# Kernel tuning notes

Hardware: AMD Instinct MI355X
Metric: run time of the kernel (lower is better)

## Reference

```python
import jax, jax.numpy as jnp
import numpy as np

A_NUM = 9
C_NUM = 20

def setup_inputs() -> dict:
    key = jax.random.key(0)
    ks = jax.random.split(key, 12)
    B, Cin, H, W = 32, 256, 56, 56
    hidden = 256
    N, M = 64, 2048
    out_ch = 5 * A_NUM + C_NUM
    features = jax.random.normal(ks[0], (B, Cin, H, W), jnp.float32)
    w1 = jax.random.normal(ks[1], (hidden, Cin), jnp.float32) * (1.0 / np.sqrt(Cin))
    b1 = jax.random.normal(ks[2], (hidden,), jnp.float32) * 0.01
    w2 = jax.random.normal(ks[3], (out_ch, hidden), jnp.float32) * (1.0 / np.sqrt(hidden))
    b2 = jax.random.normal(ks[4], (out_ch,), jnp.float32) * 0.01
    # anchor shapes (w, h), positive sizes in grid units
    anc = 1.0 + 5.0 * jax.random.uniform(ks[5], (A_NUM, 2), jnp.float32)
    # grid of cell centers
    xs = jnp.arange(W, dtype=jnp.float32) + 0.5
    ys = jnp.arange(H, dtype=jnp.float32) + 0.5
    gx, gy = jnp.meshgrid(xs, ys, indexing='xy')  # (H, W)
    grid = jnp.broadcast_to(jnp.stack([gx, gy], axis=-1)[None], (B, H, W, 2))
    # GT boxes (x1, y1, x2, y2, cls) with x1<x2, y1<y2
    x1 = jax.random.uniform(ks[6], (B, N), jnp.float32) * (W - 9.0)
    y1 = jax.random.uniform(ks[7], (B, N), jnp.float32) * (H - 9.0)
    bw = 1.0 + 7.0 * jax.random.uniform(ks[8], (B, N), jnp.float32)
    bh = 1.0 + 7.0 * jax.random.uniform(ks[9], (B, N), jnp.float32)
    cls = jax.random.randint(ks[10], (B, N), 0, C_NUM).astype(jnp.float32)
    bboxes = jnp.stack([x1, y1, x1 + bw, y1 + bh, cls], axis=-1)
    total_anchors = B * A_NUM * H * W
    pos_anchor_idx = jax.random.randint(ks[11], (M,), 0, total_anchors, jnp.int64 if jax.config.jax_enable_x64 else jnp.int32)
    neg_anchor_idx = jax.random.randint(jax.random.fold_in(key, 99), (M,), 0, total_anchors, jnp.int64 if jax.config.jax_enable_x64 else jnp.int32)
    GT_offsets = jax.random.normal(jax.random.fold_in(key, 100), (M, 4), jnp.float32) * 0.1
    return {"features": features, "w1": w1, "b1": b1, "w2": w2, "b2": b2,
            "anc": anc, "grid": grid, "bboxes": bboxes, "GT_offsets": GT_offsets,
            "pos_anchor_idx": pos_anchor_idx, "neg_anchor_idx": neg_anchor_idx}

def _generate_anchor(anc, grid):
    # grid: (B,H,W,2), anc: (A,2) -> anchors (B,A,H,W,4) as (x1,y1,x2,y2)
    g = grid[:, None]                      # (B,1,H,W,2)
    a = anc[None, :, None, None]           # (1,A,1,1,2)
    return jnp.concatenate([g - a / 2, g + a / 2], axis=-1)

def _generate_proposal_yolo(anchors, offsets):
    ctr = (anchors[..., :2] + anchors[..., 2:]) / 2
    wh = anchors[..., 2:] - anchors[..., :2]
    new_wh = wh * jnp.exp(offsets[..., 2:])
    new_ctr = ctr + offsets[..., :2]
    return jnp.concatenate([new_ctr - new_wh / 2, new_ctr + new_wh / 2], axis=-1)

def _iou(proposals, bboxes):
    # proposals (B,A,H,W,4) -> (B,AHW,4); bboxes (B,N,5) -> iou (B,AHW,N)
    B = proposals.shape[0]
    p = proposals.reshape(B, -1, 4)[:, :, None, :]   # (B,AHW,1,4)
    g = bboxes[:, None, :, :]                        # (B,1,N,5)
    ix1 = jnp.maximum(p[..., 0], g[..., 0])
    iy1 = jnp.maximum(p[..., 1], g[..., 1])
    ix2 = jnp.minimum(p[..., 2], g[..., 2])
    iy2 = jnp.minimum(p[..., 3], g[..., 3])
    inter = jnp.clip(ix2 - ix1, 0) * jnp.clip(iy2 - iy1, 0)
    gt_area = (bboxes[:, :, 2] - bboxes[:, :, 0]) * (bboxes[:, :, 3] - bboxes[:, :, 1])
    p_area = (p[..., 2] - p[..., 0]) * (p[..., 3] - p[..., 1])
    return inter / (gt_area[:, None, :] + p_area - inter)

def reference(features, w1, b1, w2, b2, anc, grid, bboxes, GT_offsets,
              pos_anchor_idx, neg_anchor_idx):
    B, _, H, W = features.shape
    A = anc.shape[0]
    M = pos_anchor_idx.shape[0]
    # PredictionNetwork (dropout in eval = identity), 1x1 convs as einsum
    x = jnp.einsum('bchw,oc->bohw', features, w1) + b1[None, :, None, None]
    x = jax.nn.leaky_relu(x, 0.01)
    x = jnp.einsum('bchw,oc->bohw', x, w2) + b2[None, :, None, None]
    anc_data = x[:, :5 * A].reshape(B, A, 5, H, W)
    class_all = x[:, 5 * A:]                               # (B,C,H,W)
    conf_all = jax.nn.sigmoid(anc_data[:, :, 0])           # (B,A,H,W)
    offsets_all = jnp.transpose(anc_data[:, :, 1:5], (0, 1, 3, 4, 2))  # (B,A,H,W,4)
    # training extraction
    conf_flat = conf_all.reshape(-1)
    conf_scores = jnp.concatenate([conf_flat[pos_anchor_idx], conf_flat[neg_anchor_idx]])[:, None]  # (2M,1)
    offsets_pos = offsets_all.reshape(-1, 4)[pos_anchor_idx]            # (M,4)
    # class scores for positive anchors: index arithmetic over (B,A,H,W)
    bi = pos_anchor_idx // (A * H * W)
    hw = pos_anchor_idx % (H * W)
    hi, wi = hw // W, hw % W
    class_pos = class_all[bi, :, hi, wi]                                # (M,C)
    # anchors -> proposals -> IoU
    anchors = _generate_anchor(anc, grid)
    proposals = _generate_proposal_yolo(anchors, offsets_all)
    iou_mat = _iou(proposals, bboxes)                                   # (B,AHW,N)
    # YOLO SSE losses
    gt_conf = jnp.concatenate([jnp.ones((M, 1), conf_scores.dtype), jnp.zeros((M, 1), conf_scores.dtype)])
    conf_loss = jnp.sum((conf_scores - gt_conf) ** 2) / (2 * M)
    reg_loss = jnp.sum((offsets_pos - GT_offsets) ** 2) / M
    total_loss = conf_loss + reg_loss
    return total_loss, iou_mat, class_pos
```

## Files before the change

kernel.cpp:

```cpp
#include <hip/hip_runtime.h>
#include <math.h>

#define B_    32
#define CIN   256
#define HID   256
#define OC    65
#define A_    9
#define H_    56
#define W_    56
#define HW    3136
#define AHW   28224
#define NBOX  64
#define M_    2048
#define CNUM  20
#define NTILE 49

#define IOU_N ((size_t)B_ * AHW * NBOX)

#define FOFF(frag) (((frag) << 3) + ((((frag) >> 3)) << 3))

typedef _Float16 half8 __attribute__((ext_vector_type(8)));
typedef float f32x16 __attribute__((ext_vector_type(16)));
typedef float f32x4  __attribute__((ext_vector_type(4)));

__device__ __forceinline__ unsigned int pkh(float a, float b) {
    _Float16 ha = (_Float16)a, hb = (_Float16)b;
    unsigned short ua = __builtin_bit_cast(unsigned short, ha);
    unsigned short ub = __builtin_bit_cast(unsigned short, hb);
    return (unsigned int)ua | ((unsigned int)ub << 16);
}

__global__ __launch_bounds__(256) void prep_kernel(
    const float* __restrict__ w1, const float* __restrict__ w2,
    _Float16* __restrict__ w1s, _Float16* __restrict__ w2s,
    float* __restrict__ loss_ws)
{
    const int f = blockIdx.x * 256 + threadIdx.x;
    if (f < 2) loss_ws[f] = 0.f;
    {
        const int e    = f & 7;
        const int lane = (f >> 3) & 63;
        const int kc   = (f >> 9) & 15;
        const int ob   = f >> 13;
        const int row  = ob * 32 + (lane & 31);
        const int k    = kc * 16 + (lane >> 5) * 8 + e;
        w1s[f] = (_Float16)w1[row * CIN + k];
    }
    if (f < 20480) {
        const int e    = f & 7;
        const int lane = (f >> 3) & 63;
        const int ks2  = (f >> 9) & 7;
        const int rt   = f >> 12;
        const int row  = rt * 16 + (lane & 15);
        const int k    = ks2 * 32 + (lane >> 4) * 8 + e;
        w2s[f] = (row < OC) ? (_Float16)w2[row * HID + k] : (_Float16)0.f;
    }
}

__global__ __launch_bounds__(256) void conv_iou_kernel(
    const float* __restrict__ features, const _Float16* __restrict__ w1s,
    const float* __restrict__ b1, const _Float16* __restrict__ w2s,
    const float* __restrict__ b2, const float* __restrict__ anc,
    const float* __restrict__ bboxes, const int* __restrict__ pos_idx,
    const int* __restrict__ neg_idx, const float* __restrict__ gt_off,
    float* __restrict__ iou_out, float* __restrict__ cls_out,
    float* __restrict__ loss_ws)
{
    __shared__ _Float16 lds_h[18432];
    __shared__ float bias_s[HID];
    __shared__ float boxs[5 * 64];
    __shared__ float red[8];

    _Float16* featAll = lds_h;
    _Float16* hidf    = lds_h;
    float*    L       = (float*)lds_h;
    float*    x2t     = L;
    float*    ppx1    = L + 4416;
    float*    ppy1    = L + 4992;
    float*    ppx2    = L + 5568;
    float*    ppy2    = L + 6144;
    float*    pare    = L + 6720;

    const int t    = threadIdx.x;
    const int lane = t & 63;
    const int w    = t >> 6;
    const int bid  = blockIdx.x;
    const int b    = bid / NTILE;
    const int p0   = (bid - b * NTILE) * 64;
    const float* fbase = features + (size_t)b * CIN * HW + p0;

    bias_s[t] = b1[t];
    if (t < 64) {
        const float* gb = bboxes + ((size_t)b * NBOX + t) * 5;
        const float x1 = gb[0], y1 = gb[1], x2v = gb[2], y2v = gb[3];
        boxs[t] = x1; boxs[64 + t] = y1; boxs[128 + t] = x2v; boxs[192 + t] = y2v;
        boxs[256 + t] = (x2v - x1) * (y2v - y1);
    }

    const int pstage = (t & 15) * 4;
    const int kk     = (t >> 4) * 2;
    const int ksS    = kk >> 4;
    const int gS     = (kk >> 3) & 1;
    const int j0h    = kk & 7;
    const int ghalf  = lane >> 5;

#pragma unroll
    for (int c = 0; c < 8; ++c) {
        const float4 r0 = *(const float4*)(fbase + (size_t)(c * 32 + kk) * HW + pstage);
        const float4 r1 = *(const float4*)(fbase + (size_t)(c * 32 + kk + 1) * HW + pstage);
        const float a0[4] = {r0.x, r0.y, r0.z, r0.w};
        const float a1[4] = {r1.x, r1.y, r1.z, r1.w};
#pragma unroll
        for (int e = 0; e < 4; ++e) {
            const int p     = pstage + e;
            const int lane2 = gS * 32 + (p & 31);
            const int pt    = p >> 5;
            const int frag  = c * 256 + (ksS * 2 + pt) * 64 + lane2;
            *(unsigned int*)&featAll[FOFF(frag) + j0h] = pkh(a0[e], a1[e]);
        }
    }
    __syncthreads();

    f32x16 facc[2][2];
#pragma unroll
    for (int ot = 0; ot < 2; ++ot)
#pragma unroll
        for (int pt = 0; pt < 2; ++pt)
#pragma unroll
            for (int e = 0; e < 16; ++e) facc[ot][pt][e] = 0.f;

    half8 afb[2][2][2];
#pragma unroll
    for (int ks = 0; ks < 2; ++ks)
#pragma unroll
        for (int ot = 0; ot < 2; ++ot)
            afb[0][ks][ot] = *(const half8*)(w1s + ((size_t)((w * 2 + ot) * 16 + ks) * 64 + lane) * 8);

#pragma unroll
    for (int c = 0; c < 8; ++c) {
        if (c < 7) {
#pragma unroll
            for (int ks = 0; ks < 2; ++ks)
#pragma unroll
                for (int ot = 0; ot < 2; ++ot)
                    afb[(c + 1) & 1][ks][ot] =
                        *(const half8*)(w1s + ((size_t)((w * 2 + ot) * 16 + (c + 1) * 2 + ks) * 64 + lane) * 8);
        }
#pragma unroll
        for (int ks = 0; ks < 2; ++ks) {
#pragma unroll
            for (int pt = 0; pt < 2; ++pt) {
                const half8 bf = *(const half8*)&featAll[FOFF(c * 256 + (ks * 2 + pt) * 64 + lane)];
                facc[0][pt] = __builtin_amdgcn_mfma_f32_32x32x16_f16(afb[c & 1][ks][0], bf, facc[0][pt], 0, 0, 0);
                facc[1][pt] = __builtin_amdgcn_mfma_f32_32x32x16_f16(afb[c & 1][ks][1], bf, facc[1][pt], 0, 0, 0);
            }
        }
    }
    __syncthreads();

    const int col = lane & 31;
#pragma unroll
    for (int ot = 0; ot < 2; ++ot) {
        const int ks2 = w * 2 + ot;
#pragma unroll
        for (int pt = 0; pt < 2; ++pt) {
            const int pt2 = pt * 2 + (col >> 4);
            const int n15 = col & 15;
#pragma unroll
            for (int q = 0; q < 4; ++q) {
                float hv[4];
#pragma unroll
                for (int i = 0; i < 4; ++i) {
                    const int row = i + 8 * q + 4 * ghalf;
                    float v = facc[ot][pt][q * 4 + i] + bias_s[w * 64 + ot * 32 + row];
                    hv[i] = v < 0.f ? 0.01f * v : v;
                }
                const int frag = (ks2 * 4 + pt2) * 64 + (q * 16 + n15);
                *(unsigned int*)&hidf[FOFF(frag) + 4 * ghalf]     = pkh(hv[0], hv[1]);
                *(unsigned int*)&hidf[FOFF(frag) + 4 * ghalf + 2] = pkh(hv[2], hv[3]);
            }
        }
    }
    __syncthreads();

    f32x4 c2[5];
#pragma unroll
    for (int rt = 0; rt < 5; ++rt)
#pragma unroll
        for (int e = 0; e < 4; ++e) c2[rt][e] = 0.f;

    const int m16 = lane & 15;
    const int kgr = lane >> 4;
#pragma unroll 2
    for (int ks2 = 0; ks2 < 8; ++ks2) {
        const half8 bf = *(const half8*)&hidf[FOFF((ks2 * 4 + w) * 64 + lane)];
#pragma unroll
        for (int rt = 0; rt < 5; ++rt) {
            const half8 af = *(const half8*)(w2s + ((size_t)(rt * 8 + ks2) * 64 + lane) * 8);
            c2[rt] = __builtin_amdgcn_mfma_f32_16x16x32_f16(af, bf, c2[rt], 0, 0, 0);
        }
    }
    __syncthreads();

    const int pxl = w * 16 + m16;
#pragma unroll
    for (int rt = 0; rt < 5; ++rt) {
#pragma unroll
        for (int r = 0; r < 4; ++r) {
            const int o2 = rt * 16 + kgr * 4 + r;
            if (o2 < OC) x2t[pxl * 69 + o2] = c2[rt][r] + b2[o2];
        }
    }
    __syncthreads();

    for (int pi = t; pi < A_ * 64; pi += 256) {
        const int a  = pi >> 6;
        const int px = pi & 63;
        const float* xr = x2t + px * 69 + 5 * a;
        const float tx = xr[1], ty = xr[2], tw = xr[3], th = xr[4];
        const int hw = p0 + px;
        const int h  = hw / W_;
        const int wv = hw - h * W_;
        const float gx = (float)wv + 0.5f;
        const float gy = (float)h + 0.5f;
        const float nw = anc[2 * a]     * __expf(tw);
        const float nh = anc[2 * a + 1] * __expf(th);
        const float cx = gx + tx, cy = gy + ty;
        ppx1[pi] = cx - 0.5f * nw; ppy1[pi] = cy - 0.5f * nh;
        ppx2[pi] = cx + 0.5f * nw; ppy2[pi] = cy + 0.5f * nh;
        pare[pi] = nw * nh;
    }
    __syncthreads();

    const int pr = lane >> 4;
    const int j0 = (lane & 15) * 4;
    float Bx1[4], By1[4], Bx2[4], By2[4], Ba[4];
#pragma unroll
    for (int e = 0; e < 4; ++e) {
        Bx1[e] = boxs[j0 + e];       By1[e] = boxs[64 + j0 + e];
        Bx2[e] = boxs[128 + j0 + e]; By2[e] = boxs[192 + j0 + e];
        Ba[e]  = boxs[256 + j0 + e];
    }
    float* ibase = iou_out + ((size_t)b * AHW + p0) * 64;
#pragma unroll 1
    for (int a = 0; a < A_; ++a) {
#pragma unroll
        for (int q = 0; q < 4; ++q) {
            const int p = w * 16 + q * 4 + pr;
            const int i = a * 64 + p;
            const float Px1 = ppx1[i], Py1 = ppy1[i], Px2 = ppx2[i], Py2 = ppy2[i];
            const float pa = pare[i];
            f32x4 o4;
#pragma unroll
            for (int e = 0; e < 4; ++e) {
                const float iw = fminf(Px2, Bx2[e]) - fmaxf(Px1, Bx1[e]);
                const float ih = fminf(Py2, By2[e]) - fmaxf(Py1, By1[e]);
                const float inter = fmaxf(iw, 0.f) * fmaxf(ih, 0.f);
                o4[e] = inter * __builtin_amdgcn_rcpf(Ba[e] + pa - inter);
            }
            __builtin_nontemporal_store(o4, (f32x4*)(ibase + ((size_t)a * HW + p) * 64 + j0));
        }
    }

    float csum = 0.f, rsum = 0.f;
    for (int m = t; m < M_; m += 256) {
        const int idx = pos_idx[m];
        const int bi  = idx / AHW;
        const int rr  = idx - bi * AHW;
        const int a   = rr / HW;
        const int px  = (rr - a * HW) - p0;
        if (bi == b && px >= 0 && px < 64) {
            const float* xr = x2t + px * 69;
            const float s = 1.f / (1.f + __expf(-xr[5 * a]));
            csum += (s - 1.f) * (s - 1.f);
#pragma unroll
            for (int k = 0; k < 4; ++k) {
                const float d = xr[5 * a + 1 + k] - gt_off[m * 4 + k];
                rsum += d * d;
            }
            float* co = cls_out + (size_t)m * CNUM;
#pragma unroll
            for (int c = 0; c < CNUM; ++c) co[c] = xr[45 + c];
        }
    }
    for (int m = t; m < M_; m += 256) {
        const int idx = neg_idx[m];
        const int bi  = idx / AHW;
        const int rr  = idx - bi * AHW;
        const int a   = rr / HW;
        const int px  = (rr - a * HW) - p0;
        if (bi == b && px >= 0 && px < 64) {
            const float s = 1.f / (1.f + __expf(-x2t[px * 69 + 5 * a]));
            csum += s * s;
        }
    }
#pragma unroll
    for (int off = 32; off > 0; off >>= 1) {
        csum += __shfl_down(csum, off, 64);
        rsum += __shfl_down(rsum, off, 64);
    }
    if (lane == 0) { red[w] = csum; red[4 + w] = rsum; }
    __syncthreads();
    if (t == 0) {
        const float c  = red[0] + red[1] + red[2] + red[3];
        const float rg = red[4] + red[5] + red[6] + red[7];
        if (c != 0.f || rg != 0.f) {
            atomicAdd(&loss_ws[0], c);
            atomicAdd(&loss_ws[1], rg);
        }
    }
}

__global__ void finalize_kernel(const float* __restrict__ loss_ws, float* __restrict__ out0)
{
    out0[0] = loss_ws[0] / (2.f * (float)M_) + loss_ws[1] / (float)M_;
}

extern "C" void kernel_launch(void* const* d_in, const int* in_sizes, int n_in,
                              void* d_out, int out_size, void* d_ws, size_t ws_size,
                              hipStream_t stream) {
    (void)in_sizes; (void)n_in; (void)out_size; (void)ws_size;
    const float* features = (const float*)d_in[0];
    const float* w1       = (const float*)d_in[1];
    const float* b1       = (const float*)d_in[2];
    const float* w2       = (const float*)d_in[3];
    const float* b2       = (const float*)d_in[4];
    const float* anc      = (const float*)d_in[5];
    const float* bboxes   = (const float*)d_in[7];
    const float* gt_off   = (const float*)d_in[8];
    const int*   pos_idx  = (const int*)d_in[9];
    const int*   neg_idx  = (const int*)d_in[10];
    float* out = (float*)d_out;

    char* wsb = (char*)d_ws;
    _Float16* w1s  = (_Float16*)wsb;
    _Float16* w2s  = w1s + 65536;
    float* loss_ws = (float*)(wsb + 131072 + 40960);

    prep_kernel<<<256, 256, 0, stream>>>(w1, w2, w1s, w2s, loss_ws);
    conv_iou_kernel<<<B_ * NTILE, 256, 0, stream>>>(features, w1s, b1, w2s, b2,
                                                    anc, bboxes, pos_idx, neg_idx,
                                                    gt_off, out + 1,
                                                    out + 1 + IOU_N, loss_ws);
    finalize_kernel<<<1, 1, 0, stream>>>(loss_ws, out);
}
```

Baseline: 379.4 us.

## Split IoU computation into separate kernel with proposals staged in workspace

Moves the IoU matrix generation out of the fused conv kernel into its own kernel launched over batch×anchor×tile blocks, with proposal boxes written to a workspace buffer in planar layout. The intent is to spread the large IoU output write across many more blocks (more memory-level parallelism) instead of 1568 blocks each serially writing nine anchor slices. It adds a kernel launch and an extra global round-trip of proposal data, and requires the workspace to hold five planes of B*A*HW floats.

```diff
diff --git a/kernel.cpp b/kernel.cpp
--- a/kernel.cpp
+++ b/kernel.cpp
@@ -15,6 +15,7 @@
 #define CNUM  20
 #define NTILE 49
 
+#define PLANE ((size_t)B_ * A_ * HW)
 #define IOU_N ((size_t)B_ * AHW * NBOX)
 
 #define FOFF(frag) (((frag) << 3) + ((((frag) >> 3)) << 3))
@@ -57,29 +58,23 @@
     }
 }
 
-__global__ __launch_bounds__(256) void conv_iou_kernel(
+__global__ __launch_bounds__(256) void conv_kernel(
     const float* __restrict__ features, const _Float16* __restrict__ w1s,
     const float* __restrict__ b1, const _Float16* __restrict__ w2s,
     const float* __restrict__ b2, const float* __restrict__ anc,
-    const float* __restrict__ bboxes, const int* __restrict__ pos_idx,
-    const int* __restrict__ neg_idx, const float* __restrict__ gt_off,
-    float* __restrict__ iou_out, float* __restrict__ cls_out,
+    const int* __restrict__ pos_idx, const int* __restrict__ neg_idx,
+    const float* __restrict__ gt_off,
+    float* __restrict__ prop, float* __restrict__ cls_out,
     float* __restrict__ loss_ws)
 {
     __shared__ _Float16 lds_h[18432];
     __shared__ float bias_s[HID];
-    __shared__ float boxs[5 * 64];
     __shared__ float red[8];
 
     _Float16* featAll = lds_h;
     _Float16* hidf    = lds_h;
     float*    L       = (float*)lds_h;
     float*    x2t     = L;
-    float*    ppx1    = L + 4416;
-    float*    ppy1    = L + 4992;
-    float*    ppx2    = L + 5568;
-    float*    ppy2    = L + 6144;
-    float*    pare    = L + 6720;
 
     const int t    = threadIdx.x;
     const int lane = t & 63;
@@ -90,12 +85,6 @@
     const float* fbase = features + (size_t)b * CIN * HW + p0;
 
     bias_s[t] = b1[t];
-    if (t < 64) {
-        const float* gb = bboxes + ((size_t)b * NBOX + t) * 5;
-        const float x1 = gb[0], y1 = gb[1], x2v = gb[2], y2v = gb[3];
-        boxs[t] = x1; boxs[64 + t] = y1; boxs[128 + t] = x2v; boxs[192 + t] = y2v;
-        boxs[256 + t] = (x2v - x1) * (y2v - y1);
-    }
 
     const int pstage = (t & 15) * 4;
     const int kk     = (t >> 4) * 2;
@@ -226,40 +215,12 @@
         const float nw = anc[2 * a]     * __expf(tw);
         const float nh = anc[2 * a + 1] * __expf(th);
         const float cx = gx + tx, cy = gy + ty;
-        ppx1[pi] = cx - 0.5f * nw; ppy1[pi] = cy - 0.5f * nh;
-        ppx2[pi] = cx + 0.5f * nw; ppy2[pi] = cy + 0.5f * nh;
-        pare[pi] = nw * nh;
-    }
-    __syncthreads();
-
-    const int pr = lane >> 4;
-    const int j0 = (lane & 15) * 4;
-    float Bx1[4], By1[4], Bx2[4], By2[4], Ba[4];
-#pragma unroll
-    for (int e = 0; e < 4; ++e) {
-        Bx1[e] = boxs[j0 + e];       By1[e] = boxs[64 + j0 + e];
-        Bx2[e] = boxs[128 + j0 + e]; By2[e] = boxs[192 + j0 + e];
-        Ba[e]  = boxs[256 + j0 + e];
-    }
-    float* ibase = iou_out + ((size_t)b * AHW + p0) * 64;
-#pragma unroll 1
-    for (int a = 0; a < A_; ++a) {
-#pragma unroll
-        for (int q = 0; q < 4; ++q) {
-            const int p = w * 16 + q * 4 + pr;
-            const int i = a * 64 + p;
-            const float Px1 = ppx1[i], Py1 = ppy1[i], Px2 = ppx2[i], Py2 = ppy2[i];
-            const float pa = pare[i];
-            f32x4 o4;
-#pragma unroll
-            for (int e = 0; e < 4; ++e) {
-                const float iw = fminf(Px2, Bx2[e]) - fmaxf(Px1, Bx1[e]);
-                const float ih = fminf(Py2, By2[e]) - fmaxf(Py1, By1[e]);
-                const float inter = fmaxf(iw, 0.f) * fmaxf(ih, 0.f);
-                o4[e] = inter * __builtin_amdgcn_rcpf(Ba[e] + pa - inter);
-            }
-            __builtin_nontemporal_store(o4, (f32x4*)(ibase + ((size_t)a * HW + p) * 64 + j0));
-        }
+        const size_t pb = ((size_t)b * A_ + a) * HW + p0 + px;
+        prop[pb]             = cx - 0.5f * nw;
+        prop[PLANE + pb]     = cy - 0.5f * nh;
+        prop[2 * PLANE + pb] = cx + 0.5f * nw;
+        prop[3 * PLANE + pb] = cy + 0.5f * nh;
+        prop[4 * PLANE + pb] = nw * nh;
     }
 
     float csum = 0.f, rsum = 0.f;
@@ -308,6 +269,64 @@
             atomicAdd(&loss_ws[0], c);
             atomicAdd(&loss_ws[1], rg);
         }
+    }
+}
+
+__global__ __launch_bounds__(256) void iou_kernel(
+    const float* __restrict__ prop, const float* __restrict__ bboxes,
+    float* __restrict__ iou_out)
+{
+    __shared__ float P[5 * 64];
+    __shared__ float boxs[5 * 64];
+
+    const int t    = threadIdx.x;
+    const int lane = t & 63;
+    const int w    = t >> 6;
+    const int bid  = blockIdx.x;
+    const int b    = bid / (A_ * NTILE);
+    const int r    = bid - b * (A_ * NTILE);
+    const int a    = r / NTILE;
+    const int p0   = (r - a * NTILE) * 64;
+
+    const size_t pbase = ((size_t)b * A_ + a) * HW + p0;
+
+    if (t < 64) {
+        const float* gb = bboxes + ((size_t)b * NBOX + t) * 5;
+        const float x1 = gb[0], y1 = gb[1], x2v = gb[2], y2v = gb[3];
+        boxs[t] = x1; boxs[64 + t] = y1; boxs[128 + t] = x2v; boxs[192 + t] = y2v;
+        boxs[256 + t] = (x2v - x1) * (y2v - y1);
+    }
+    for (int i = t; i < 320; i += 256) {
+        const int s = i >> 6;
+        P[i] = prop[(size_t)s * PLANE + pbase + (i & 63)];
+    }
+    __syncthreads();
+
+    const int pr = lane >> 4;
+    const int j0 = (lane & 15) * 4;
+    float Bx1[4], By1[4], Bx2[4], By2[4], Ba[4];
+#pragma unroll
+    for (int e = 0; e < 4; ++e) {
+        Bx1[e] = boxs[j0 + e];       By1[e] = boxs[64 + j0 + e];
+        Bx2[e] = boxs[128 + j0 + e]; By2[e] = boxs[192 + j0 + e];
+        Ba[e]  = boxs[256 + j0 + e];
+    }
+
+    float* ibase = iou_out + pbase * 64;
+#pragma unroll
+    for (int q = 0; q < 4; ++q) {
+        const int p = w * 16 + q * 4 + pr;
+        const float Px1 = P[p], Py1 = P[64 + p], Px2 = P[128 + p], Py2 = P[192 + p];
+        const float pa  = P[256 + p];
+        f32x4 o4;
+#pragma unroll
+        for (int e = 0; e < 4; ++e) {
+            const float iw = fminf(Px2, Bx2[e]) - fmaxf(Px1, Bx1[e]);
+            const float ih = fminf(Py2, By2[e]) - fmaxf(Py1, By1[e]);
+            const float inter = fmaxf(iw, 0.f) * fmaxf(ih, 0.f);
+            o4[e] = inter * __builtin_amdgcn_rcpf(Ba[e] + pa - inter);
+        }
+        __builtin_nontemporal_store(o4, (f32x4*)(ibase + (size_t)p * 64 + j0));
     }
 }
 
@@ -336,11 +355,12 @@
     _Float16* w1s  = (_Float16*)wsb;
     _Float16* w2s  = w1s + 65536;
     float* loss_ws = (float*)(wsb + 131072 + 40960);
+    float* prop    = (float*)(wsb + 172288);
 
     prep_kernel<<<256, 256, 0, stream>>>(w1, w2, w1s, w2s, loss_ws);
-    conv_iou_kernel<<<B_ * NTILE, 256, 0, stream>>>(features, w1s, b1, w2s, b2,
-                                                    anc, bboxes, pos_idx, neg_idx,
-                                                    gt_off, out + 1,
-                                                    out + 1 + IOU_N, loss_ws);
+    conv_kernel<<<B_ * NTILE, 256, 0, stream>>>(features, w1s, b1, w2s, b2, anc,
+                                                pos_idx, neg_idx, gt_off,
+                                                prop, out + 1 + IOU_N, loss_ws);
+    iou_kernel<<<B_ * A_ * NTILE, 256, 0, stream>>>(prop, bboxes, out + 1);
     finalize_kernel<<<1, 1, 0, stream>>>(loss_ws, out);
 }
```

Result: slower. 389.9 us (+2.8%).

## Make each wave own 16 pixels end-to-end, removing shared staging and block barriers

Applied to the files above, without the earlier changes.

The first 1x1 conv now uses 16x16x32 MFMAs. Each wave loads its own 16 pixels of features straight into registers, so the shared-memory feature staging is gone. Every later stage (hidden activations, head output, proposals, IoU) uses per-wave LDS regions, which removes most __syncthreads between stages. The LDS footprint shrinks and launch bounds request 3 blocks per CU to raise occupancy. The trade-off is strided scalar global loads for features, 16 accumulator tiles per wave that increase register pressure, and IoU stores that are no longer nontemporal.

```diff
diff --git a/kernel.cpp b/kernel.cpp
--- a/kernel.cpp
+++ b/kernel.cpp
@@ -17,10 +17,7 @@
 
 #define IOU_N ((size_t)B_ * AHW * NBOX)
 
-#define FOFF(frag) (((frag) << 3) + ((((frag) >> 3)) << 3))
-
 typedef _Float16 half8 __attribute__((ext_vector_type(8)));
-typedef float f32x16 __attribute__((ext_vector_type(16)));
 typedef float f32x4  __attribute__((ext_vector_type(4)));
 
 __device__ __forceinline__ unsigned int pkh(float a, float b) {
@@ -40,10 +37,10 @@
     {
         const int e    = f & 7;
         const int lane = (f >> 3) & 63;
-        const int kc   = (f >> 9) & 15;
-        const int ob   = f >> 13;
-        const int row  = ob * 32 + (lane & 31);
-        const int k    = kc * 16 + (lane >> 5) * 8 + e;
+        const int ks   = (f >> 9) & 7;
+        const int rt   = (f >> 12) & 15;
+        const int row  = rt * 16 + (lane & 15);
+        const int k    = ks * 32 + (lane >> 4) * 8 + e;
         w1s[f] = (_Float16)w1[row * CIN + k];
     }
     if (f < 20480) {
@@ -57,7 +54,7 @@
     }
 }
 
-__global__ __launch_bounds__(256) void conv_iou_kernel(
+__global__ __launch_bounds__(256, 3) void conv_iou_kernel(
     const float* __restrict__ features, const _Float16* __restrict__ w1s,
     const float* __restrict__ b1, const _Float16* __restrict__ w2s,
     const float* __restrict__ b2, const float* __restrict__ anc,
@@ -66,122 +63,67 @@
     float* __restrict__ iou_out, float* __restrict__ cls_out,
     float* __restrict__ loss_ws)
 {
-    __shared__ _Float16 lds_h[18432];
-    __shared__ float bias_s[HID];
-    __shared__ float boxs[5 * 64];
+    __shared__ _Float16 lds_h[16384];
     __shared__ float red[8];
 
-    _Float16* featAll = lds_h;
-    _Float16* hidf    = lds_h;
-    float*    L       = (float*)lds_h;
-    float*    x2t     = L;
-    float*    ppx1    = L + 4416;
-    float*    ppy1    = L + 4992;
-    float*    ppx2    = L + 5568;
-    float*    ppy2    = L + 6144;
-    float*    pare    = L + 6720;
+    float* LF = (float*)lds_h;
 
     const int t    = threadIdx.x;
     const int lane = t & 63;
     const int w    = t >> 6;
+    const int pxw  = lane & 15;
+    const int g    = lane >> 4;
     const int bid  = blockIdx.x;
     const int b    = bid / NTILE;
     const int p0   = (bid - b * NTILE) * 64;
-    const float* fbase = features + (size_t)b * CIN * HW + p0;
-
-    bias_s[t] = b1[t];
-    if (t < 64) {
-        const float* gb = bboxes + ((size_t)b * NBOX + t) * 5;
-        const float x1 = gb[0], y1 = gb[1], x2v = gb[2], y2v = gb[3];
-        boxs[t] = x1; boxs[64 + t] = y1; boxs[128 + t] = x2v; boxs[192 + t] = y2v;
-        boxs[256 + t] = (x2v - x1) * (y2v - y1);
-    }
-
-    const int pstage = (t & 15) * 4;
-    const int kk     = (t >> 4) * 2;
-    const int ksS    = kk >> 4;
-    const int gS     = (kk >> 3) & 1;
-    const int j0h    = kk & 7;
-    const int ghalf  = lane >> 5;
-
-#pragma unroll
-    for (int c = 0; c < 8; ++c) {
-        const float4 r0 = *(const float4*)(fbase + (size_t)(c * 32 + kk) * HW + pstage);
-        const float4 r1 = *(const float4*)(fbase + (size_t)(c * 32 + kk + 1) * HW + pstage);
-        const float a0[4] = {r0.x, r0.y, r0.z, r0.w};
-        const float a1[4] = {r1.x, r1.y, r1.z, r1.w};
-#pragma unroll
-        for (int e = 0; e < 4; ++e) {
-            const int p     = pstage + e;
-            const int lane2 = gS * 32 + (p & 31);
-            const int pt    = p >> 5;
-            const int frag  = c * 256 + (ksS * 2 + pt) * 64 + lane2;
-            *(unsigned int*)&featAll[FOFF(frag) + j0h] = pkh(a0[e], a1[e]);
-        }
-    }
-    __syncthreads();
-
-    f32x16 facc[2][2];
-#pragma unroll
-    for (int ot = 0; ot < 2; ++ot)
-#pragma unroll
-        for (int pt = 0; pt < 2; ++pt)
-#pragma unroll
-            for (int e = 0; e < 16; ++e) facc[ot][pt][e] = 0.f;
-
-    half8 afb[2][2][2];
-#pragma unroll
-    for (int ks = 0; ks < 2; ++ks)
-#pragma unroll
-        for (int ot = 0; ot < 2; ++ot)
-            afb[0][ks][ot] = *(const half8*)(w1s + ((size_t)((w * 2 + ot) * 16 + ks) * 64 + lane) * 8);
-
-#pragma unroll
-    for (int c = 0; c < 8; ++c) {
-        if (c < 7) {
-#pragma unroll
-            for (int ks = 0; ks < 2; ++ks)
-#pragma unroll
-                for (int ot = 0; ot < 2; ++ot)
-                    afb[(c + 1) & 1][ks][ot] =
-                        *(const half8*)(w1s + ((size_t)((w * 2 + ot) * 16 + (c + 1) * 2 + ks) * 64 + lane) * 8);
-        }
-#pragma unroll
-        for (int ks = 0; ks < 2; ++ks) {
-#pragma unroll
-            for (int pt = 0; pt < 2; ++pt) {
-                const half8 bf = *(const half8*)&featAll[FOFF(c * 256 + (ks * 2 + pt) * 64 + lane)];
-                facc[0][pt] = __builtin_amdgcn_mfma_f32_32x32x16_f16(afb[c & 1][ks][0], bf, facc[0][pt], 0, 0, 0);
-                facc[1][pt] = __builtin_amdgcn_mfma_f32_32x32x16_f16(afb[c & 1][ks][1], bf, facc[1][pt], 0, 0, 0);
-            }
-        }
-    }
-    __syncthreads();
-
-    const int col = lane & 31;
-#pragma unroll
-    for (int ot = 0; ot < 2; ++ot) {
-        const int ks2 = w * 2 + ot;
-#pragma unroll
-        for (int pt = 0; pt < 2; ++pt) {
-            const int pt2 = pt * 2 + (col >> 4);
-            const int n15 = col & 15;
-#pragma unroll
-            for (int q = 0; q < 4; ++q) {
-                float hv[4];
-#pragma unroll
-                for (int i = 0; i < 4; ++i) {
-                    const int row = i + 8 * q + 4 * ghalf;
-                    float v = facc[ot][pt][q * 4 + i] + bias_s[w * 64 + ot * 32 + row];
-                    hv[i] = v < 0.f ? 0.01f * v : v;
-                }
-                const int frag = (ks2 * 4 + pt2) * 64 + (q * 16 + n15);
-                *(unsigned int*)&hidf[FOFF(frag) + 4 * ghalf]     = pkh(hv[0], hv[1]);
-                *(unsigned int*)&hidf[FOFF(frag) + 4 * ghalf + 2] = pkh(hv[2], hv[3]);
-            }
-        }
-    }
-    __syncthreads();
+
+    const float* fpx = features + (size_t)b * CIN * HW + (p0 + w * 16 + pxw);
+    half8 b1f[8];
+#pragma unroll
+    for (int ks = 0; ks < 8; ++ks) {
+        float v[8];
+#pragma unroll
+        for (int j = 0; j < 8; ++j)
+            v[j] = fpx[(size_t)(ks * 32 + g * 8 + j) * HW];
+#pragma unroll
+        for (int j = 0; j < 8; ++j)
+            b1f[ks][j] = (_Float16)v[j];
+    }
+
+    f32x4 facc[16];
+#pragma unroll
+    for (int rt = 0; rt < 16; ++rt)
+#pragma unroll
+        for (int e = 0; e < 4; ++e) facc[rt][e] = 0.f;
+
+#pragma unroll
+    for (int ks = 0; ks < 8; ++ks) {
+#pragma unroll
+        for (int rt = 0; rt < 16; ++rt) {
+            const half8 af = *(const half8*)(w1s + ((size_t)(rt * 8 + ks) * 64 + lane) * 8);
+            facc[rt] = __builtin_amdgcn_mfma_f32_16x16x32_f16(af, b1f[ks], facc[rt], 0, 0, 0);
+        }
+    }
+
+    _Float16* wreg_h = lds_h + w * 4096;
+#pragma unroll
+    for (int rt = 0; rt < 16; ++rt) {
+        const int hb = rt * 16 + g * 4;
+        const float4 b4 = *(const float4*)(b1 + hb);
+        const float bb[4] = {b4.x, b4.y, b4.z, b4.w};
+        float hv[4];
+#pragma unroll
+        for (int r = 0; r < 4; ++r) {
+            const float v = facc[rt][r] + bb[r];
+            hv[r] = v < 0.f ? 0.01f * v : v;
+        }
+        const int ks2   = hb >> 5;
+        const int e0    = hb & 7;
+        const int lane2 = ((hb >> 3) & 3) * 16 + pxw;
+        const int ah    = ks2 * 512 + lane2 * 8 + e0;
+        *(unsigned int*)&wreg_h[ah]     = pkh(hv[0], hv[1]);
+        *(unsigned int*)&wreg_h[ah + 2] = pkh(hv[2], hv[3]);
+    }
 
     f32x4 c2[5];
 #pragma unroll
@@ -189,67 +131,72 @@
 #pragma unroll
         for (int e = 0; e < 4; ++e) c2[rt][e] = 0.f;
 
-    const int m16 = lane & 15;
-    const int kgr = lane >> 4;
-#pragma unroll 2
+#pragma unroll
     for (int ks2 = 0; ks2 < 8; ++ks2) {
-        const half8 bf = *(const half8*)&hidf[FOFF((ks2 * 4 + w) * 64 + lane)];
+        const half8 bf = *(const half8*)&wreg_h[ks2 * 512 + lane * 8];
 #pragma unroll
         for (int rt = 0; rt < 5; ++rt) {
             const half8 af = *(const half8*)(w2s + ((size_t)(rt * 8 + ks2) * 64 + lane) * 8);
             c2[rt] = __builtin_amdgcn_mfma_f32_16x16x32_f16(af, bf, c2[rt], 0, 0, 0);
         }
     }
-    __syncthreads();
-
-    const int pxl = w * 16 + m16;
+    asm volatile("" ::: "memory");
+
+    float* xw = LF + w * 2048 + 768;
 #pragma unroll
     for (int rt = 0; rt < 5; ++rt) {
-#pragma unroll
-        for (int r = 0; r < 4; ++r) {
-            const int o2 = rt * 16 + kgr * 4 + r;
-            if (o2 < OC) x2t[pxl * 69 + o2] = c2[rt][r] + b2[o2];
-        }
-    }
-    __syncthreads();
-
-    for (int pi = t; pi < A_ * 64; pi += 256) {
-        const int a  = pi >> 6;
-        const int px = pi & 63;
-        const float* xr = x2t + px * 69 + 5 * a;
+        const int ob = rt * 16 + g * 4;
+        if (rt < 4) {
+            const float4 b4 = *(const float4*)(b2 + ob);
+            const float bb[4] = {b4.x, b4.y, b4.z, b4.w};
+#pragma unroll
+            for (int r = 0; r < 4; ++r)
+                xw[pxw * 69 + ob + r] = c2[rt][r] + bb[r];
+        } else if (g == 0) {
+            xw[pxw * 69 + 64] = c2[4][0] + b2[64];
+        }
+    }
+
+    float* WP = LF + w * 2048;
+    for (int i = lane; i < A_ * 16; i += 64) {
+        const int a  = i >> 4;
+        const int pw = i & 15;
+        const float* xr = xw + pw * 69 + 5 * a;
         const float tx = xr[1], ty = xr[2], tw = xr[3], th = xr[4];
-        const int hw = p0 + px;
-        const int h  = hw / W_;
-        const int wv = hw - h * W_;
+        const int hwg = p0 + w * 16 + pw;
+        const int h   = hwg / W_;
+        const int wv  = hwg - h * W_;
         const float gx = (float)wv + 0.5f;
         const float gy = (float)h + 0.5f;
         const float nw = anc[2 * a]     * __expf(tw);
         const float nh = anc[2 * a + 1] * __expf(th);
         const float cx = gx + tx, cy = gy + ty;
-        ppx1[pi] = cx - 0.5f * nw; ppy1[pi] = cy - 0.5f * nh;
-        ppx2[pi] = cx + 0.5f * nw; ppy2[pi] = cy + 0.5f * nh;
-        pare[pi] = nw * nh;
-    }
-    __syncthreads();
+        WP[i]       = cx - 0.5f * nw;
+        WP[144 + i] = cy - 0.5f * nh;
+        WP[288 + i] = cx + 0.5f * nw;
+        WP[432 + i] = cy + 0.5f * nh;
+        WP[576 + i] = nw * nh;
+    }
 
     const int pr = lane >> 4;
     const int j0 = (lane & 15) * 4;
     float Bx1[4], By1[4], Bx2[4], By2[4], Ba[4];
 #pragma unroll
     for (int e = 0; e < 4; ++e) {
-        Bx1[e] = boxs[j0 + e];       By1[e] = boxs[64 + j0 + e];
-        Bx2[e] = boxs[128 + j0 + e]; By2[e] = boxs[192 + j0 + e];
-        Ba[e]  = boxs[256 + j0 + e];
+        const float* gb = bboxes + ((size_t)b * NBOX + j0 + e) * 5;
+        Bx1[e] = gb[0]; By1[e] = gb[1]; Bx2[e] = gb[2]; By2[e] = gb[3];
+        Ba[e]  = (gb[2] - gb[0]) * (gb[3] - gb[1]);
     }
     float* ibase = iou_out + ((size_t)b * AHW + p0) * 64;
 #pragma unroll 1
     for (int a = 0; a < A_; ++a) {
 #pragma unroll
         for (int q = 0; q < 4; ++q) {
-            const int p = w * 16 + q * 4 + pr;
-            const int i = a * 64 + p;
-            const float Px1 = ppx1[i], Py1 = ppy1[i], Px2 = ppx2[i], Py2 = ppy2[i];
-            const float pa = pare[i];
+            const int pw  = q * 4 + pr;
+            const int idx = a * 16 + pw;
+            const float Px1 = WP[idx],       Py1 = WP[144 + idx];
+            const float Px2 = WP[288 + idx], Py2 = WP[432 + idx];
+            const float pa  = WP[576 + idx];
             f32x4 o4;
 #pragma unroll
             for (int e = 0; e < 4; ++e) {
@@ -258,9 +205,11 @@
                 const float inter = fmaxf(iw, 0.f) * fmaxf(ih, 0.f);
                 o4[e] = inter * __builtin_amdgcn_rcpf(Ba[e] + pa - inter);
             }
-            __builtin_nontemporal_store(o4, (f32x4*)(ibase + ((size_t)a * HW + p) * 64 + j0));
-        }
-    }
+            *(f32x4*)(ibase + ((size_t)(a * HW) + w * 16 + pw) * 64 + j0) = o4;
+        }
+    }
+
+    __syncthreads();
 
     float csum = 0.f, rsum = 0.f;
     for (int m = t; m < M_; m += 256) {
@@ -270,7 +219,7 @@
         const int a   = rr / HW;
         const int px  = (rr - a * HW) - p0;
         if (bi == b && px >= 0 && px < 64) {
-            const float* xr = x2t + px * 69;
+            const float* xr = LF + ((px >> 4) * 2048 + 768 + (px & 15) * 69);
             const float s = 1.f / (1.f + __expf(-xr[5 * a]));
             csum += (s - 1.f) * (s - 1.f);
 #pragma unroll
@@ -290,7 +239,7 @@
         const int a   = rr / HW;
         const int px  = (rr - a * HW) - p0;
         if (bi == b && px >= 0 && px < 64) {
-            const float s = 1.f / (1.f + __expf(-x2t[px * 69 + 5 * a]));
+            const float s = 1.f / (1.f + __expf(-LF[(px >> 4) * 2048 + 768 + (px & 15) * 69 + 5 * a]));
             csum += s * s;
         }
     }
```

New measurement: 446.7 us. 17.7% more time.
